# Performance work log

Measured on AMD Instinct MI355X. Metric: run time of the kernel, lower is better.

## Reference

```python
import jax, jax.numpy as jnp
import numpy as np

N_NODES = 100000
N_EDGES = 1600000
IN_FEATS = 256
HIDDEN = 128
N_CLASSES = 128
NEG_SLOPE = 0.2


def setup_inputs() -> dict:
    key = jax.random.key(0)
    ks = jax.random.split(key, 12)
    inp = {
        "features": jax.random.normal(ks[0], (N_NODES, IN_FEATS), dtype=jnp.float32),
        "src": jax.random.randint(ks[1], (N_EDGES,), 0, N_NODES, dtype=jnp.int32),
        "dst": jax.random.randint(ks[2], (N_EDGES,), 0, N_NODES, dtype=jnp.int32),
        # layer 1 params (Xavier-ish scale)
        "W1": jax.random.normal(ks[3], (HIDDEN, IN_FEATS), dtype=jnp.float32) / np.sqrt(IN_FEATS),
        "al1": jax.random.normal(ks[4], (HIDDEN,), dtype=jnp.float32) / np.sqrt(HIDDEN),
        "ar1": jax.random.normal(ks[5], (HIDDEN,), dtype=jnp.float32) / np.sqrt(HIDDEN),
        "b1": jnp.zeros((HIDDEN,), dtype=jnp.float32),
        # layer 2 params
        "W2": jax.random.normal(ks[6], (N_CLASSES, HIDDEN), dtype=jnp.float32) / np.sqrt(HIDDEN),
        "al2": jax.random.normal(ks[7], (N_CLASSES,), dtype=jnp.float32) / np.sqrt(N_CLASSES),
        "ar2": jax.random.normal(ks[8], (N_CLASSES,), dtype=jnp.float32) / np.sqrt(N_CLASSES),
        "b2": jnp.zeros((N_CLASSES,), dtype=jnp.float32),
    }
    return inp


def _gat_conv(x, W, attn_l, attn_r, bias, src, dst):
    """Single-head DGL GATConv: fc -> edge leaky-relu scores -> segment softmax over dst -> scatter-sum."""
    h = x @ W.T                                   # [N, D]
    el = h @ attn_l                               # [N]
    er = h @ attn_r                               # [N]
    e = jax.nn.leaky_relu(el[src] + er[dst], NEG_SLOPE)   # [E]
    # numerically stable segment softmax over incoming edges of each dst node
    m = jax.ops.segment_max(e, dst, num_segments=N_NODES)          # [N] (-inf for empty)
    ex = jnp.exp(e - m[dst])                                       # [E]
    s = jax.ops.segment_sum(ex, dst, num_segments=N_NODES)         # [N]
    alpha = ex / s[dst]                                            # [E]
    out = jax.ops.segment_sum(h[src] * alpha[:, None], dst, num_segments=N_NODES)
    return out + bias


def reference(features, src, dst, W1, al1, ar1, b1, W2, al2, ar2, b2):
    x = _gat_conv(features, W1, al1, ar1, b1, src, dst)
    x = jax.nn.elu(x)
    return _gat_conv(x, W2, al2, ar2, b2, src, dst)
```

## Files before the change

### kernel.cpp

```cpp
#include <hip/hip_runtime.h>

typedef unsigned short u16;
typedef unsigned int u32;

#define NEG_SLOPE 0.2f
#define BSHIFT 8
#define MAXBUCK 1024

using short8 = __attribute__((ext_vector_type(8))) short;
using float4v = __attribute__((ext_vector_type(4))) float;
using float2v = __attribute__((ext_vector_type(2))) float;

__device__ __forceinline__ float bfu(u16 v) { return __uint_as_float(((u32)v) << 16); }
__device__ __forceinline__ float bflo(u32 u) { return __uint_as_float(u << 16); }
__device__ __forceinline__ float bfhi(u32 u) { return __uint_as_float(u & 0xffff0000u); }
__device__ __forceinline__ u16 f2bf(float f) {
  u32 x = __float_as_uint(f);
  return (u16)((x + 0x7fffu + ((x >> 16) & 1u)) >> 16);
}
__device__ __forceinline__ float loadf(const void* p, int idx, int isbf) {
  return isbf ? bfu(((const u16*)p)[idx]) : ((const float*)p)[idx];
}

__global__ __launch_bounds__(256) void detect_dtype(const u32* __restrict__ w,
                                                    int nwords, int* __restrict__ flag) {
  __shared__ int cnt;
  if (threadIdx.x == 0) cnt = 0;
  __syncthreads();
  int c = 0;
  for (int i = threadIdx.x; i < nwords; i += 256) {
    u32 e = (w[i] >> 7) & 0xFFu;
    c += (e >= 0x60u && e <= 0x90u) ? 1 : 0;
  }
  atomicAdd(&cnt, c);
  __syncthreads();
  if (threadIdx.x == 0) flag[0] = (cnt * 2 > nwords) ? 1 : 0;
}

__global__ __launch_bounds__(256) void scanA(int* __restrict__ a,
                                             int* __restrict__ bsum, int M) {
  __shared__ int sh[256];
  int t = threadIdx.x;
  int idx = blockIdx.x * 256 + t;
  int v = (idx < M) ? a[idx] : 0;
  sh[t] = v;
  __syncthreads();
  for (int off = 1; off < 256; off <<= 1) {
    int y = (t >= off) ? sh[t - off] : 0;
    __syncthreads();
    sh[t] += y;
    __syncthreads();
  }
  if (idx < M) a[idx] = sh[t] - v;
  if (t == 255) bsum[blockIdx.x] = sh[255];
}

__global__ __launch_bounds__(512) void scanBseq(int* __restrict__ a, int MB) {
  __shared__ int sh[512];
  __shared__ int carry;
  int t = threadIdx.x;
  if (t == 0) carry = 0;
  __syncthreads();
  for (int base = 0; base < MB; base += 512) {
    int v = (base + t < MB) ? a[base + t] : 0;
    sh[t] = v;
    __syncthreads();
    for (int off = 1; off < 512; off <<= 1) {
      int y = (t >= off) ? sh[t - off] : 0;
      __syncthreads();
      sh[t] += y;
      __syncthreads();
    }
    int c0 = carry;
    int excl = sh[t] - v + c0;
    int tot = sh[511];
    __syncthreads();
    if (t == 0) carry = c0 + tot;
    if (base + t < MB) a[base + t] = excl;
    __syncthreads();
  }
}

__global__ __launch_bounds__(256) void part_scatter(const int* __restrict__ src,
                                                    const int* __restrict__ dst,
                                                    const int* __restrict__ Gh,
                                                    const int* __restrict__ bsumA,
                                                    int* __restrict__ pd,
                                                    int* __restrict__ ps,
                                                    int E, int PB, int nbuck) {
  __shared__ int cur[MAXBUCK];
  int t = threadIdx.x;
  int blk = blockIdx.x;
  for (int i = t; i < nbuck; i += 256) {
    int j = i * PB + blk;
    cur[i] = Gh[j] + bsumA[j >> 8];
  }
  __syncthreads();
  int pbase = blk * 4096;
#pragma unroll
  for (int j = 0; j < 16; ++j) {
    int e = pbase + j * 256 + t;
    if (e < E) {
      int d = dst[e];
      int s = src[e];
      u32 b = (u32)d >> BSHIFT;
      if (b < (u32)nbuck) {
        int slot = atomicAdd(&cur[b], 1);
        if ((u32)slot < (u32)E) {
          pd[slot] = d;
          ps[slot] = s;
        }
      }
    }
  }
}

__global__ __launch_bounds__(256) void bucket_sort(const int* __restrict__ pd,
                                                   const int* __restrict__ ps,
                                                   const int* __restrict__ Gh,
                                                   const int* __restrict__ bsumA,
                                                   int* __restrict__ indptr,
                                                   int* __restrict__ ssrc,
                                                   int E, int N, int PB, int nbuck) {
  __shared__ int bins[256];
  __shared__ int sh[256];
  __shared__ int cur[256];
  int t = threadIdx.x;
  int b = blockIdx.x;
  int j0 = b * PB;
  int base = Gh[j0] + bsumA[j0 >> 8];
  int nextb = E;
  if (b + 1 < nbuck) {
    int j1 = (b + 1) * PB;
    nextb = Gh[j1] + bsumA[j1 >> 8];
  }
  int sz = nextb - base;

  bins[t] = 0;
  __syncthreads();
  for (int i = t; i < sz; i += 256) atomicAdd(&bins[pd[base + i] & 255], 1);
  __syncthreads();

  int v = bins[t];
  sh[t] = v;
  __syncthreads();
  for (int off = 1; off < 256; off <<= 1) {
    int y = (t >= off) ? sh[t - off] : 0;
    __syncthreads();
    sh[t] += y;
    __syncthreads();
  }
  int excl = sh[t] - v;
  int node = b * 256 + t;
  if (node < N) indptr[node] = base + excl;
  if (b == 0 && t == 0) indptr[N] = E;
  cur[t] = excl;
  __syncthreads();

  for (int i = t; i < sz; i += 256) {
    int d = pd[base + i];
    int slot = atomicAdd(&cur[d & 255], 1);
    u32 gidx = (u32)(base + slot);
    if (gidx < (u32)E) ssrc[gidx] = ps[base + i];
  }
}

__global__ __launch_bounds__(256) void bsw_build(const void* __restrict__ W,
                                                 u16* __restrict__ Bsw, int K,
                                                 const int* __restrict__ dflag) {
  const int isbf = dflag[0];
  int t = blockIdx.x * 256 + threadIdx.x;
  int total = (K / 32) * 8 * 64;
  if (t >= total) return;
  int lane = t & 63;
  int c = (t >> 6) & 7;
  int ktile = t >> 9;
  int n = lane & 15, q = lane >> 4;
  int col = c * 16 + n;
  u16 vals[8];
#pragma unroll
  for (int j = 0; j < 8; ++j) {
    int k = ktile * 32 + q * 8 + j;
    int idx = col * K + k;
    vals[j] = isbf ? ((const u16*)W)[idx] : f2bf(((const float*)W)[idx]);
  }
  *(uint4*)(Bsw + (size_t)t * 8) = *(uint4*)vals;
}

template <int K, int ISBF>
__device__ __forceinline__ void gemm_core(const void* __restrict__ Xv,
                                          const u16* __restrict__ Bsw,
                                          const int* mclamp, int q, int lane,
                                          float4v acc[2][8]) {
  constexpr int NT = K / 32;
  const uint4* btb = (const uint4*)Bsw + lane;
  if (ISBF) {
    const u16* X0 = (const u16*)Xv + (size_t)mclamp[0] * K + q * 8;
    const u16* X1 = (const u16*)Xv + (size_t)mclamp[1] * K + q * 8;
    short8 a0[NT], a1[NT];
#pragma unroll
    for (int t = 0; t < NT; ++t) a0[t] = *(const short8*)(X0 + t * 32);
#pragma unroll
    for (int t = 0; t < NT; ++t) a1[t] = *(const short8*)(X1 + t * 32);
#pragma unroll
    for (int t = 0; t < NT; ++t) {
      const uint4* bt = btb + (size_t)t * 8 * 64;
#pragma unroll
      for (int c = 0; c < 8; ++c) {
        uint4 bw = bt[c * 64];
        short8 bf = *(short8*)&bw;
        acc[0][c] = __builtin_amdgcn_mfma_f32_16x16x32_bf16(a0[t], bf, acc[0][c], 0, 0, 0);
        acc[1][c] = __builtin_amdgcn_mfma_f32_16x16x32_bf16(a1[t], bf, acc[1][c], 0, 0, 0);
      }
    }
  } else {
    const float* X0 = (const float*)Xv + (size_t)mclamp[0] * K + q * 8;
    const float* X1 = (const float*)Xv + (size_t)mclamp[1] * K + q * 8;
    float4 f00 = *(const float4*)X0, f01 = *(const float4*)(X0 + 4);
    float4 f10 = *(const float4*)X1, f11 = *(const float4*)(X1 + 4);
#pragma unroll
    for (int t = 0; t < NT; ++t) {
      float4 g00 = f00, g01 = f01, g10 = f10, g11 = f11;
      if (t + 1 < NT) {
        g00 = *(const float4*)(X0 + (t + 1) * 32);
        g01 = *(const float4*)(X0 + (t + 1) * 32 + 4);
        g10 = *(const float4*)(X1 + (t + 1) * 32);
        g11 = *(const float4*)(X1 + (t + 1) * 32 + 4);
      }
      u16 t0[8] = {f2bf(f00.x), f2bf(f00.y), f2bf(f00.z), f2bf(f00.w),
                   f2bf(f01.x), f2bf(f01.y), f2bf(f01.z), f2bf(f01.w)};
      u16 t1[8] = {f2bf(f10.x), f2bf(f10.y), f2bf(f10.z), f2bf(f10.w),
                   f2bf(f11.x), f2bf(f11.y), f2bf(f11.z), f2bf(f11.w)};
      short8 a0 = *(short8*)t0;
      short8 a1 = *(short8*)t1;
      const uint4* bt = btb + (size_t)t * 8 * 64;
#pragma unroll
      for (int c = 0; c < 8; ++c) {
        uint4 bw = bt[c * 64];
        short8 bf = *(short8*)&bw;
        acc[0][c] = __builtin_amdgcn_mfma_f32_16x16x32_bf16(a0, bf, acc[0][c], 0, 0, 0);
        acc[1][c] = __builtin_amdgcn_mfma_f32_16x16x32_bf16(a1, bf, acc[1][c], 0, 0, 0);
      }
      f00 = g00; f01 = g01; f10 = g10; f11 = g11;
    }
  }
}

template <int K, int DYNA>
__device__ __forceinline__ void gemm_body(int bix, const void* __restrict__ Xv,
                                          const u16* __restrict__ Bsw,
                                          u16* __restrict__ Hb,
                                          const void* __restrict__ al,
                                          const void* __restrict__ ar,
                                          float* __restrict__ el_,
                                          float* __restrict__ er_, int N,
                                          const int* __restrict__ dflag) {
  const int isbfP = dflag[0];
  int tid = threadIdx.x;
  int w = tid >> 6, lane = tid & 63;
  int n = lane & 15, q = lane >> 4;
  int base = bix * 128 + w * 32;

  int mclamp[2];
#pragma unroll
  for (int mt = 0; mt < 2; ++mt) {
    int m = base + mt * 16 + n;
    mclamp[mt] = (m < N) ? m : 0;
  }

  float alv[8], arv[8];
#pragma unroll
  for (int c = 0; c < 8; ++c) {
    alv[c] = loadf(al, c * 16 + n, isbfP);
    arv[c] = loadf(ar, c * 16 + n, isbfP);
  }

  float4v acc[2][8];
#pragma unroll
  for (int mt = 0; mt < 2; ++mt)
#pragma unroll
    for (int c = 0; c < 8; ++c) acc[mt][c] = (float4v){0.f, 0.f, 0.f, 0.f};

  if (DYNA == 0 || isbfP) {
    gemm_core<K, 1>(Xv, Bsw, mclamp, q, lane, acc);
  } else {
    gemm_core<K, 0>(Xv, Bsw, mclamp, q, lane, acc);
  }

#pragma unroll
  for (int mt = 0; mt < 2; ++mt)
#pragma unroll
    for (int c = 0; c < 8; ++c) {
#pragma unroll
      for (int r = 0; r < 4; ++r) {
        int row = base + mt * 16 + q * 4 + r;
        if (row < N) Hb[(size_t)row * 128 + c * 16 + n] = f2bf(acc[mt][c][r]);
      }
    }

#pragma unroll
  for (int mt = 0; mt < 2; ++mt)
#pragma unroll
    for (int r = 0; r < 4; ++r) {
      float sl = 0.f, sr = 0.f;
#pragma unroll
      for (int c = 0; c < 8; ++c) {
        float v = acc[mt][c][r];
        sl = fmaf(v, alv[c], sl);
        sr = fmaf(v, arv[c], sr);
      }
#pragma unroll
      for (int off = 1; off < 16; off <<= 1) {
        sl += __shfl_xor(sl, off);
        sr += __shfl_xor(sr, off);
      }
      if (n == 0) {
        int row = base + mt * 16 + q * 4 + r;
        if (row < N) {
          el_[row] = sl;
          er_[row] = sr;
        }
      }
    }
}

template <int K, int DYNA>
__global__ __launch_bounds__(256) void gemm_mfma(const void* __restrict__ Xv,
                                                 const u16* __restrict__ Bsw,
                                                 u16* __restrict__ Hb,
                                                 const void* __restrict__ al,
                                                 const void* __restrict__ ar,
                                                 float* __restrict__ el_,
                                                 float* __restrict__ er_, int N,
                                                 const int* __restrict__ dflag) {
  gemm_body<K, DYNA>(blockIdx.x, Xv, Bsw, Hb, al, ar, el_, er_, N, dflag);
}

template <int K, int DYNA>
__global__ __launch_bounds__(256) void fused_gemm_hist(
    const void* __restrict__ Xv, const u16* __restrict__ Bsw, u16* __restrict__ Hb,
    const void* __restrict__ al, const void* __restrict__ ar,
    float* __restrict__ el_, float* __restrict__ er_, int N,
    const int* __restrict__ dflag, int gemm_blocks,
    const int* __restrict__ dst, int* __restrict__ Gh, int E, int PB, int nbuck) {
  __shared__ int hcnt[MAXBUCK];
  int bix = (int)blockIdx.x;
  if (bix < gemm_blocks) {
    gemm_body<K, DYNA>(bix, Xv, Bsw, Hb, al, ar, el_, er_, N, dflag);
    return;
  }
  int pblk = bix - gemm_blocks;
  int t = threadIdx.x;
  for (int i = t; i < nbuck; i += 256) hcnt[i] = 0;
  __syncthreads();
  int pbase = pblk * 4096;
#pragma unroll
  for (int j = 0; j < 16; ++j) {
    int e = pbase + j * 256 + t;
    if (e < E) {
      u32 b = (u32)dst[e] >> BSHIFT;
      if (b < (u32)nbuck) atomicAdd(&hcnt[b], 1);
    }
  }
  __syncthreads();
  for (int i = t; i < nbuck; i += 256) Gh[(size_t)i * PB + pblk] = hcnt[i];
}

template <int MODE>
__global__ __launch_bounds__(256) void agg_kernel(const u32* __restrict__ Hb,
                                                  const float* __restrict__ el,
                                                  const float* __restrict__ er,
                                                  const int* __restrict__ indptr,
                                                  const int* __restrict__ ssrc,
                                                  const void* __restrict__ bias,
                                                  void* __restrict__ outv, int N,
                                                  const int* __restrict__ dflag) {
  const int isbf = dflag[0];
  int tid = threadIdx.x;
  int n = blockIdx.x * 4 + (tid >> 6);
  int lane = tid & 63;
  if (n >= N) return;

  int beg = indptr[n];
  int end = indptr[n + 1];
  int deg = end - beg;
  float ern = er[n];

  float2v acc = {0.f, 0.f};
  float inv;

  if (deg <= 64) {
    int valid = lane < deg;
    int ide = valid ? ssrc[beg + lane] : 0;
    float sc = el[ide] + ern;
    sc = (sc > 0.f) ? sc : NEG_SLOPE * sc;
    sc = valid ? sc : -INFINITY;

    float m = sc;
#pragma unroll
    for (int off = 1; off < 64; off <<= 1) m = fmaxf(m, __shfl_xor(m, off));
    float pe = __expf(sc - m);
    float l = pe;
#pragma unroll
    for (int off = 1; off < 64; off <<= 1) l += __shfl_xor(l, off);

    int e = 0;
    for (; e + 8 <= deg; e += 8) {
      int id_[8];
      u32 h_[8];
#pragma unroll
      for (int k = 0; k < 8; ++k) id_[k] = __builtin_amdgcn_readlane(ide, e + k);
#pragma unroll
      for (int k = 0; k < 8; ++k) h_[k] = Hb[(size_t)id_[k] * 64 + lane];
#pragma unroll
      for (int k = 0; k < 8; ++k) {
        float pk = __int_as_float(__builtin_amdgcn_readlane(__float_as_int(pe), e + k));
        float2v hv = {bflo(h_[k]), bfhi(h_[k])};
        float2v pv = {pk, pk};
        acc = pv * hv + acc;
      }
    }
    for (; e + 4 <= deg; e += 4) {
      int id_[4];
      u32 h_[4];
#pragma unroll
      for (int k = 0; k < 4; ++k) id_[k] = __builtin_amdgcn_readlane(ide, e + k);
#pragma unroll
      for (int k = 0; k < 4; ++k) h_[k] = Hb[(size_t)id_[k] * 64 + lane];
#pragma unroll
      for (int k = 0; k < 4; ++k) {
        float pk = __int_as_float(__builtin_amdgcn_readlane(__float_as_int(pe), e + k));
        float2v hv = {bflo(h_[k]), bfhi(h_[k])};
        float2v pv = {pk, pk};
        acc = pv * hv + acc;
      }
    }
    for (; e < deg; ++e) {
      int i0 = __builtin_amdgcn_readlane(ide, e);
      u32 h0 = Hb[(size_t)i0 * 64 + lane];
      float pk = __int_as_float(__builtin_amdgcn_readlane(__float_as_int(pe), e));
      float2v hv = {bflo(h0), bfhi(h0)};
      float2v pv = {pk, pk};
      acc = pv * hv + acc;
    }
    inv = (deg > 0 && l > 0.f) ? 1.f / l : 0.f;
  } else {
    float m_run = -INFINITY, l_run = 0.f;
    for (int p = beg; p < end; p += 64) {
      int rem = end - p;
      int valid = lane < rem;
      int ide = valid ? ssrc[p + lane] : 0;
      float sc = el[ide] + ern;
      sc = (sc > 0.f) ? sc : NEG_SLOPE * sc;
      sc = valid ? sc : -INFINITY;
      float mc = sc;
#pragma unroll
      for (int off = 1; off < 64; off <<= 1) mc = fmaxf(mc, __shfl_xor(mc, off));
      float m_new = fmaxf(m_run, mc);
      float corr = __expf(m_run - m_new);
      float pe = __expf(sc - m_new);
      float ls = pe;
#pragma unroll
      for (int off = 1; off < 64; off <<= 1) ls += __shfl_xor(ls, off);
      l_run = l_run * corr + ls;
      float2v cv = {corr, corr};
      acc = acc * cv;
      m_run = m_new;

      int cl = (rem < 64) ? rem : 64;
      int e = 0;
      for (; e + 8 <= cl; e += 8) {
        int id_[8];
        u32 h_[8];
#pragma unroll
        for (int k = 0; k < 8; ++k) id_[k] = __builtin_amdgcn_readlane(ide, e + k);
#pragma unroll
        for (int k = 0; k < 8; ++k) h_[k] = Hb[(size_t)id_[k] * 64 + lane];
#pragma unroll
        for (int k = 0; k < 8; ++k) {
          float pk = __int_as_float(__builtin_amdgcn_readlane(__float_as_int(pe), e + k));
          float2v hv = {bflo(h_[k]), bfhi(h_[k])};
          float2v pv = {pk, pk};
          acc = pv * hv + acc;
        }
      }
      for (; e < cl; ++e) {
        int i0 = __builtin_amdgcn_readlane(ide, e);
        u32 h0 = Hb[(size_t)i0 * 64 + lane];
        float pk = __int_as_float(__builtin_amdgcn_readlane(__float_as_int(pe), e));
        float2v hv = {bflo(h0), bfhi(h0)};
        float2v pv = {pk, pk};
        acc = pv * hv + acc;
      }
    }
    inv = (l_run > 0.f) ? 1.f / l_run : 0.f;
  }

  float o0 = acc.x * inv + loadf(bias, 2 * lane, isbf);
  float o1 = acc.y * inv + loadf(bias, 2 * lane + 1, isbf);

  if (MODE == 0) {
    o0 = (o0 > 0.f) ? o0 : (__expf(o0) - 1.f);
    o1 = (o1 > 0.f) ? o1 : (__expf(o1) - 1.f);
    ((u32*)outv)[(size_t)n * 64 + lane] = (u32)f2bf(o0) | ((u32)f2bf(o1) << 16);
  } else {
    if (isbf) {
      ((u32*)outv)[(size_t)n * 64 + lane] = (u32)f2bf(o0) | ((u32)f2bf(o1) << 16);
    } else {
      ((float2*)outv)[(size_t)n * 64 + lane] = make_float2(o0, o1);
    }
  }
}


extern "C" void kernel_launch(void* const* d_in, const int* in_sizes, int n_in,
                              void* d_out, int out_size, void* d_ws, size_t ws_size,
                              hipStream_t stream) {
  const int IN_FEATS = 256, HID = 128;
  const void* features = d_in[0];
  const int* src = (const int*)d_in[1];
  const int* dst = (const int*)d_in[2];
  const void* W1 = d_in[3];
  const void* al1 = d_in[4];
  const void* ar1 = d_in[5];
  const void* b1 = d_in[6];
  const void* W2 = d_in[7];
  const void* al2 = d_in[8];
  const void* ar2 = d_in[9];
  const void* b2 = d_in[10];

  const int N = in_sizes[0] / IN_FEATS;
  const int E = in_sizes[1];

  char* p = (char*)d_ws;
  auto alloc = [&](size_t bytes) -> void* {
    void* q = (void*)p;
    p += (bytes + 255) & ~(size_t)255;
    return q;
  };
  int* dflag = (int*)alloc(256);
  u16* Bsw1 = (u16*)alloc((size_t)(IN_FEATS / 32) * 8 * 64 * 8 * 2);
  u16* Bsw2 = (u16*)alloc((size_t)(HID / 32) * 8 * 64 * 8 * 2);
  u16* hb = (u16*)alloc((size_t)N * HID * 2);
  u16* x = (u16*)alloc((size_t)N * HID * 2);
  float* el = (float*)alloc((size_t)N * 4);
  float* er = (float*)alloc((size_t)N * 4);
  int* indptr = (int*)alloc((size_t)(N + 1) * 4);

  const int nbuck = (N + 255) >> BSHIFT;
  const int PB = (E + 4095) / 4096;
  const int M = nbuck * PB;
  const int MB1 = (M + 255) / 256;

  int* Gh = (int*)alloc((size_t)M * 4);
  int* bsumA = (int*)alloc((size_t)MB1 * 4);
  int* ssrc = (int*)alloc((size_t)E * 4);

  int* pd = (int*)x;
  int* ps = (int*)((char*)x + (((size_t)E * 4 + 255) & ~(size_t)255));

  const int GEMM_B = (N + 127) / 128;
  const int NODE_B = (N + 3) / 4;

  detect_dtype<<<1, 256, 0, stream>>>((const u32*)features, 4096, dflag);
  bsw_build<<<((IN_FEATS / 32) * 8 * 64 + 255) / 256, 256, 0, stream>>>(W1, Bsw1, IN_FEATS, dflag);
  bsw_build<<<((HID / 32) * 8 * 64 + 255) / 256, 256, 0, stream>>>(W2, Bsw2, HID, dflag);

  fused_gemm_hist<IN_FEATS, 1><<<GEMM_B + PB, 256, 0, stream>>>(
      features, Bsw1, hb, al1, ar1, el, er, N, dflag, GEMM_B, dst, Gh, E, PB, nbuck);

  scanA<<<MB1, 256, 0, stream>>>(Gh, bsumA, M);
  scanBseq<<<1, 512, 0, stream>>>(bsumA, MB1);

  part_scatter<<<PB, 256, 0, stream>>>(src, dst, Gh, bsumA, pd, ps, E, PB, nbuck);
  bucket_sort<<<nbuck, 256, 0, stream>>>(pd, ps, Gh, bsumA, indptr, ssrc, E, N, PB, nbuck);

  agg_kernel<0><<<NODE_B, 256, 0, stream>>>((const u32*)hb, el, er, indptr, ssrc, b1, (void*)x, N, dflag);

  gemm_mfma<HID, 0><<<GEMM_B, 256, 0, stream>>>((const void*)x, Bsw2, hb, al2, ar2, el, er, N, dflag);
  agg_kernel<1><<<NODE_B, 256, 0, stream>>>((const u32*)hb, el, er, indptr, ssrc, b2, d_out, N, dflag);
}
```

Before: 463.8 us.

## Pack partition pairs into one word, vectorize edge loads, tweak GEMM and gather addressing

After: 418.7 us. -9.7%, faster.

```diff
diff --git a/kernel.cpp b/kernel.cpp
--- a/kernel.cpp
+++ b/kernel.cpp
@@ -85,8 +85,7 @@
                                                     const int* __restrict__ dst,
                                                     const int* __restrict__ Gh,
                                                     const int* __restrict__ bsumA,
-                                                    int* __restrict__ pd,
-                                                    int* __restrict__ ps,
+                                                    u32* __restrict__ pp,
                                                     int E, int PB, int nbuck) {
   __shared__ int cur[MAXBUCK];
   int t = threadIdx.x;
@@ -98,25 +97,41 @@
   __syncthreads();
   int pbase = blk * 4096;
 #pragma unroll
-  for (int j = 0; j < 16; ++j) {
-    int e = pbase + j * 256 + t;
-    if (e < E) {
-      int d = dst[e];
-      int s = src[e];
-      u32 b = (u32)d >> BSHIFT;
-      if (b < (u32)nbuck) {
-        int slot = atomicAdd(&cur[b], 1);
-        if ((u32)slot < (u32)E) {
-          pd[slot] = d;
-          ps[slot] = s;
+  for (int j = 0; j < 4; ++j) {
+    int e = pbase + (j * 256 + t) * 4;
+    if (e + 3 < E) {
+      int4 dv = *(const int4*)(dst + e);
+      int4 sv = *(const int4*)(src + e);
+      int dd[4] = {dv.x, dv.y, dv.z, dv.w};
+      int ss[4] = {sv.x, sv.y, sv.z, sv.w};
+#pragma unroll
+      for (int k = 0; k < 4; ++k) {
+        u32 b = (u32)dd[k] >> BSHIFT;
+        if (b < (u32)nbuck) {
+          int slot = atomicAdd(&cur[b], 1);
+          if ((u32)slot < (u32)E)
+            pp[slot] = (u32)ss[k] | (((u32)dd[k] & 255u) << 24);
         }
       }
-    }
-  }
-}
-
-__global__ __launch_bounds__(256) void bucket_sort(const int* __restrict__ pd,
-                                                   const int* __restrict__ ps,
+    } else {
+      for (int k = 0; k < 4; ++k) {
+        int ee = e + k;
+        if (ee < E) {
+          int d = dst[ee];
+          int s = src[ee];
+          u32 b = (u32)d >> BSHIFT;
+          if (b < (u32)nbuck) {
+            int slot = atomicAdd(&cur[b], 1);
+            if ((u32)slot < (u32)E)
+              pp[slot] = (u32)s | (((u32)d & 255u) << 24);
+          }
+        }
+      }
+    }
+  }
+}
+
+__global__ __launch_bounds__(256) void bucket_sort(const u32* __restrict__ pp,
                                                    const int* __restrict__ Gh,
                                                    const int* __restrict__ bsumA,
                                                    int* __restrict__ indptr,
@@ -138,7 +153,7 @@
 
   bins[t] = 0;
   __syncthreads();
-  for (int i = t; i < sz; i += 256) atomicAdd(&bins[pd[base + i] & 255], 1);
+  for (int i = t; i < sz; i += 256) atomicAdd(&bins[pp[base + i] >> 24], 1);
   __syncthreads();
 
   int v = bins[t];
@@ -158,10 +173,10 @@
   __syncthreads();
 
   for (int i = t; i < sz; i += 256) {
-    int d = pd[base + i];
-    int slot = atomicAdd(&cur[d & 255], 1);
+    u32 w = pp[base + i];
+    int slot = atomicAdd(&cur[w >> 24], 1);
     u32 gidx = (u32)(base + slot);
-    if (gidx < (u32)E) ssrc[gidx] = ps[base + i];
+    if (gidx < (u32)E) ssrc[gidx] = (int)(w & 0x00FFFFFFu);
   }
 }
 
@@ -202,6 +217,7 @@
     for (int t = 0; t < NT; ++t) a0[t] = *(const short8*)(X0 + t * 32);
 #pragma unroll
     for (int t = 0; t < NT; ++t) a1[t] = *(const short8*)(X1 + t * 32);
+    __builtin_amdgcn_sched_barrier(0);
 #pragma unroll
     for (int t = 0; t < NT; ++t) {
       const uint4* bt = btb + (size_t)t * 8 * 64;
@@ -325,19 +341,19 @@
 }
 
 template <int K, int DYNA>
-__global__ __launch_bounds__(256) void gemm_mfma(const void* __restrict__ Xv,
-                                                 const u16* __restrict__ Bsw,
-                                                 u16* __restrict__ Hb,
-                                                 const void* __restrict__ al,
-                                                 const void* __restrict__ ar,
-                                                 float* __restrict__ el_,
-                                                 float* __restrict__ er_, int N,
-                                                 const int* __restrict__ dflag) {
+__global__ __launch_bounds__(256, 1) void gemm_mfma(const void* __restrict__ Xv,
+                                                    const u16* __restrict__ Bsw,
+                                                    u16* __restrict__ Hb,
+                                                    const void* __restrict__ al,
+                                                    const void* __restrict__ ar,
+                                                    float* __restrict__ el_,
+                                                    float* __restrict__ er_, int N,
+                                                    const int* __restrict__ dflag) {
   gemm_body<K, DYNA>(blockIdx.x, Xv, Bsw, Hb, al, ar, el_, er_, N, dflag);
 }
 
 template <int K, int DYNA>
-__global__ __launch_bounds__(256) void fused_gemm_hist(
+__global__ __launch_bounds__(256, 1) void fused_gemm_hist(
     const void* __restrict__ Xv, const u16* __restrict__ Bsw, u16* __restrict__ Hb,
     const void* __restrict__ al, const void* __restrict__ ar,
     float* __restrict__ el_, float* __restrict__ er_, int N,
@@ -355,11 +371,24 @@
   __syncthreads();
   int pbase = pblk * 4096;
 #pragma unroll
-  for (int j = 0; j < 16; ++j) {
-    int e = pbase + j * 256 + t;
-    if (e < E) {
-      u32 b = (u32)dst[e] >> BSHIFT;
-      if (b < (u32)nbuck) atomicAdd(&hcnt[b], 1);
+  for (int j = 0; j < 4; ++j) {
+    int e = pbase + (j * 256 + t) * 4;
+    if (e + 3 < E) {
+      int4 dv = *(const int4*)(dst + e);
+      int dd[4] = {dv.x, dv.y, dv.z, dv.w};
+#pragma unroll
+      for (int k = 0; k < 4; ++k) {
+        u32 b = (u32)dd[k] >> BSHIFT;
+        if (b < (u32)nbuck) atomicAdd(&hcnt[b], 1);
+      }
+    } else {
+      for (int k = 0; k < 4; ++k) {
+        int ee = e + k;
+        if (ee < E) {
+          u32 b = (u32)dst[ee] >> BSHIFT;
+          if (b < (u32)nbuck) atomicAdd(&hcnt[b], 1);
+        }
+      }
     }
   }
   __syncthreads();
@@ -381,6 +410,8 @@
   int lane = tid & 63;
   if (n >= N) return;
 
+  const char* hbase = (const char*)Hb + ((u32)lane << 2);
+
   int beg = indptr[n];
   int end = indptr[n + 1];
   int deg = end - beg;
@@ -392,6 +423,7 @@
   if (deg <= 64) {
     int valid = lane < deg;
     int ide = valid ? ssrc[beg + lane] : 0;
+    ide = (u32)ide < (u32)N ? ide : 0;
     float sc = el[ide] + ern;
     sc = (sc > 0.f) ? sc : NEG_SLOPE * sc;
     sc = valid ? sc : -INFINITY;
@@ -406,12 +438,13 @@
 
     int e = 0;
     for (; e + 8 <= deg; e += 8) {
-      int id_[8];
+      u32 off_[8];
       u32 h_[8];
 #pragma unroll
-      for (int k = 0; k < 8; ++k) id_[k] = __builtin_amdgcn_readlane(ide, e + k);
-#pragma unroll
-      for (int k = 0; k < 8; ++k) h_[k] = Hb[(size_t)id_[k] * 64 + lane];
+      for (int k = 0; k < 8; ++k)
+        off_[k] = (u32)__builtin_amdgcn_readlane(ide, e + k) << 8;
+#pragma unroll
+      for (int k = 0; k < 8; ++k) h_[k] = *(const u32*)(hbase + off_[k]);
 #pragma unroll
       for (int k = 0; k < 8; ++k) {
         float pk = __int_as_float(__builtin_amdgcn_readlane(__float_as_int(pe), e + k));
@@ -421,12 +454,13 @@
       }
     }
     for (; e + 4 <= deg; e += 4) {
-      int id_[4];
+      u32 off_[4];
       u32 h_[4];
 #pragma unroll
-      for (int k = 0; k < 4; ++k) id_[k] = __builtin_amdgcn_readlane(ide, e + k);
-#pragma unroll
-      for (int k = 0; k < 4; ++k) h_[k] = Hb[(size_t)id_[k] * 64 + lane];
+      for (int k = 0; k < 4; ++k)
+        off_[k] = (u32)__builtin_amdgcn_readlane(ide, e + k) << 8;
+#pragma unroll
+      for (int k = 0; k < 4; ++k) h_[k] = *(const u32*)(hbase + off_[k]);
 #pragma unroll
       for (int k = 0; k < 4; ++k) {
         float pk = __int_as_float(__builtin_amdgcn_readlane(__float_as_int(pe), e + k));
@@ -436,8 +470,8 @@
       }
     }
     for (; e < deg; ++e) {
-      int i0 = __builtin_amdgcn_readlane(ide, e);
-      u32 h0 = Hb[(size_t)i0 * 64 + lane];
+      u32 off0 = (u32)__builtin_amdgcn_readlane(ide, e) << 8;
+      u32 h0 = *(const u32*)(hbase + off0);
       float pk = __int_as_float(__builtin_amdgcn_readlane(__float_as_int(pe), e));
       float2v hv = {bflo(h0), bfhi(h0)};
       float2v pv = {pk, pk};
@@ -450,6 +484,7 @@
       int rem = end - p;
       int valid = lane < rem;
       int ide = valid ? ssrc[p + lane] : 0;
+      ide = (u32)ide < (u32)N ? ide : 0;
       float sc = el[ide] + ern;
       sc = (sc > 0.f) ? sc : NEG_SLOPE * sc;
       sc = valid ? sc : -INFINITY;
@@ -470,12 +505,13 @@
       int cl = (rem < 64) ? rem : 64;
       int e = 0;
       for (; e + 8 <= cl; e += 8) {
-        int id_[8];
+        u32 off_[8];
         u32 h_[8];
 #pragma unroll
-        for (int k = 0; k < 8; ++k) id_[k] = __builtin_amdgcn_readlane(ide, e + k);
-#pragma unroll
-        for (int k = 0; k < 8; ++k) h_[k] = Hb[(size_t)id_[k] * 64 + lane];
+        for (int k = 0; k < 8; ++k)
+          off_[k] = (u32)__builtin_amdgcn_readlane(ide, e + k) << 8;
+#pragma unroll
+        for (int k = 0; k < 8; ++k) h_[k] = *(const u32*)(hbase + off_[k]);
 #pragma unroll
         for (int k = 0; k < 8; ++k) {
           float pk = __int_as_float(__builtin_amdgcn_readlane(__float_as_int(pe), e + k));
@@ -485,8 +521,8 @@
         }
       }
       for (; e < cl; ++e) {
-        int i0 = __builtin_amdgcn_readlane(ide, e);
-        u32 h0 = Hb[(size_t)i0 * 64 + lane];
+        u32 off0 = (u32)__builtin_amdgcn_readlane(ide, e) << 8;
+        u32 h0 = *(const u32*)(hbase + off0);
         float pk = __int_as_float(__builtin_amdgcn_readlane(__float_as_int(pe), e));
         float2v hv = {bflo(h0), bfhi(h0)};
         float2v pv = {pk, pk};
@@ -556,8 +592,7 @@
   int* bsumA = (int*)alloc((size_t)MB1 * 4);
   int* ssrc = (int*)alloc((size_t)E * 4);
 
-  int* pd = (int*)x;
-  int* ps = (int*)((char*)x + (((size_t)E * 4 + 255) & ~(size_t)255));
+  u32* pp = (u32*)x;
 
   const int GEMM_B = (N + 127) / 128;
   const int NODE_B = (N + 3) / 4;
@@ -572,8 +607,8 @@
   scanA<<<MB1, 256, 0, stream>>>(Gh, bsumA, M);
   scanBseq<<<1, 512, 0, stream>>>(bsumA, MB1);
 
-  part_scatter<<<PB, 256, 0, stream>>>(src, dst, Gh, bsumA, pd, ps, E, PB, nbuck);
-  bucket_sort<<<nbuck, 256, 0, stream>>>(pd, ps, Gh, bsumA, indptr, ssrc, E, N, PB, nbuck);
+  part_scatter<<<PB, 256, 0, stream>>>(src, dst, Gh, bsumA, pp, E, PB, nbuck);
+  bucket_sort<<<nbuck, 256, 0, stream>>>(pp, Gh, bsumA, indptr, ssrc, E, N, PB, nbuck);
 
   agg_kernel<0><<<NODE_B, 256, 0, stream>>>((const u32*)hb, el, er, indptr, ssrc, b1, (void*)x, N, dflag);
 
```
